# Kernel tuning notes

Measured on AMD Instinct MI355X. Metric: run time of the kernel, lower is better.

## Reference

```python
import jax, jax.numpy as jnp
import numpy as np
from jax import lax

B, C, H, W, D, V = 1, 32, 128, 160, 64, 5


def _make_projs():
    # proj_matrices[b, v, 0] = 4x4 extrinsics [R|t], proj_matrices[b, v, 1] = 4x4 intrinsics
    f = 800.0
    K = np.eye(4, dtype=np.float32)
    K[0, 0] = K[1, 1] = f
    K[0, 2] = W / 2.0
    K[1, 2] = H / 2.0
    projs = np.zeros((B, V, 2, 4, 4), np.float32)
    for b in range(B):
        for v in range(V):
            E = np.eye(4, dtype=np.float32)
            if v > 0:
                ang = 0.02 * v
                ca, sa = np.cos(ang), np.sin(ang)
                E[:3, :3] = np.array([[ca, 0.0, sa], [0.0, 1.0, 0.0], [-sa, 0.0, ca]], np.float32)
                E[:3, 3] = np.array([0.1 * v, 0.02 * v, 0.05 * v], np.float32)
            projs[b, v, 0] = E
            projs[b, v, 1] = K
    return jnp.asarray(projs)


def setup_inputs() -> dict:
    key = jax.random.key(0)
    ks = jax.random.split(key, 6)
    inp = {f"feat{i}": jax.random.normal(ks[i], (B, C, H, W), jnp.float32) for i in range(V)}
    inp["proj_matrices"] = _make_projs()
    inp["depth_values"] = jnp.broadcast_to(
        jnp.linspace(425.0, 935.0, D, dtype=jnp.float32)[None, :], (B, D))
    inp["num_depth"] = D
    inp["conv_w"] = jax.random.normal(ks[5], (1, C, 3, 3, 3), jnp.float32) * 0.05
    inp["conv_b"] = jnp.zeros((1,), jnp.float32)
    return inp


def _bilinear_sample(fea, px, py):
    # fea: [B,C,H,W]; px,py: [B,N] pixel coords. Bilinear, zero padding, align_corners=True.
    Bb, Cc, Hh, Ww = fea.shape
    fea_flat = fea.reshape(Bb, Cc, Hh * Ww)
    x0 = jnp.floor(px)
    y0 = jnp.floor(py)
    wx1 = px - x0
    wy1 = py - y0

    def corner(xc, yc, w):
        valid = (xc >= 0) & (xc <= Ww - 1) & (yc >= 0) & (yc <= Hh - 1)
        xi = jnp.clip(xc, 0, Ww - 1).astype(jnp.int32)
        yi = jnp.clip(yc, 0, Hh - 1).astype(jnp.int32)
        idx = yi * Ww + xi  # [B,N]
        g = jax.vmap(lambda fb, ib: fb[:, ib])(fea_flat, idx)  # [B,C,N]
        return g * (w * valid)[:, None, :]

    return (corner(x0, y0, (1 - wx1) * (1 - wy1))
            + corner(x0 + 1, y0, wx1 * (1 - wy1))
            + corner(x0, y0 + 1, (1 - wx1) * wy1)
            + corner(x0 + 1, y0 + 1, wx1 * wy1))


def _homo_warp(src_fea, src_proj, ref_proj, depth_values):
    # homo_warping_3D: warp src features into ref frustum at each depth hypothesis
    Bb, Cc, Hh, Ww = src_fea.shape
    Dd = depth_values.shape[1]
    proj = jnp.einsum('bij,bjk->bik', src_proj, jnp.linalg.inv(ref_proj))
    rot, trans = proj[:, :3, :3], proj[:, :3, 3]
    yy, xx = jnp.meshgrid(jnp.arange(Hh, dtype=src_fea.dtype),
                          jnp.arange(Ww, dtype=src_fea.dtype), indexing='ij')
    xyz = jnp.stack([xx.ravel(), yy.ravel(), jnp.ones(Hh * Ww, src_fea.dtype)])  # [3,HW]
    rot_xyz = jnp.einsum('bij,jn->bin', rot, xyz)  # [B,3,HW]
    pxyz = rot_xyz[:, :, None, :] * depth_values[:, None, :, None] + trans[:, :, None, None]  # [B,3,D,HW]
    px = (pxyz[:, 0] / pxyz[:, 2]).reshape(Bb, -1)
    py = (pxyz[:, 1] / pxyz[:, 2]).reshape(Bb, -1)
    return _bilinear_sample(src_fea, px, py).reshape(Bb, Cc, Dd, Hh, Ww)


def _fuse_proj(p):
    # p: [B,2,4,4] -> [B,4,4] with K[:3,:3] @ E[:3,:4] written into top 3 rows
    top = jnp.einsum('bij,bjk->bik', p[:, 1, :3, :3], p[:, 0, :3, :4])
    return p[:, 0].at[:, :3, :4].set(top)


def reference(feat0, feat1, feat2, feat3, feat4, proj_matrices, depth_values, num_depth, conv_w, conv_b):
    feats = [feat0, feat1, feat2, feat3, feat4]
    num_views = len(feats)
    Bb, Cc, Hh, Ww = feat0.shape
    ref_proj = _fuse_proj(proj_matrices[:, 0])
    ref_vol = jnp.broadcast_to(feat0[:, :, None, :, :], (Bb, Cc, num_depth, Hh, Ww))
    vol_sum = ref_vol
    vol_sq = ref_vol ** 2
    for v in range(1, num_views):
        src_proj = _fuse_proj(proj_matrices[:, v])
        warped = _homo_warp(feats[v], src_proj, ref_proj, depth_values)
        vol_sum = vol_sum + warped
        vol_sq = vol_sq + warped ** 2
    variance = vol_sq / num_views - (vol_sum / num_views) ** 2  # [B,C,D,H,W]
    cost = lax.conv_general_dilated(variance, conv_w, (1, 1, 1), 'SAME',
                                    dimension_numbers=('NCDHW', 'OIDHW', 'NCDHW'))
    cost = cost + conv_b[None, :, None, None, None]
    prob_volume_pre = cost[:, 0]  # squeeze channel -> [B,D,H,W]
    return jax.nn.softmax(prob_volume_pre, axis=1)
```

## Files before the change

### kernel.cpp

```cpp
#include <hip/hip_runtime.h>

#define H_ 128
#define W_ 160
#define C_ 32
#define D_ 64
#define HW_ (H_*W_)
#define DHW_ (D_*HW_)

#define TY 16
#define TX 16
#define HS 18
#define NP_ (HS*HS)
#define PCHUNK 81

#define GSTR 28

#define FEATT_SZ (5*HW_*C_)
#define MATS_OFF FEATT_SZ
#define CW3_OFF (MATS_OFF + 64)
#define A_OFF (CW3_OFF + 1152)

using v2f = __attribute__((ext_vector_type(2))) float;

__device__ __forceinline__ v2f pk_mul(v2f a, v2f b) {
    v2f d; asm("v_pk_mul_f32 %0, %1, %2" : "=v"(d) : "v"(a), "v"(b)); return d;
}
__device__ __forceinline__ v2f pk_add(v2f a, v2f b) {
    v2f d; asm("v_pk_add_f32 %0, %1, %2" : "=v"(d) : "v"(a), "v"(b)); return d;
}
__device__ __forceinline__ v2f pk_fma(v2f a, v2f b, v2f c) {
    v2f d; asm("v_pk_fma_f32 %0, %1, %2, %3" : "=v"(d) : "v"(a), "v"(b), "v"(c)); return d;
}
__device__ __forceinline__ v2f pk_mul_blo(v2f a, v2f b) {
    v2f d; asm("v_pk_mul_f32 %0, %1, %2 op_sel:[0,0] op_sel_hi:[1,0]" : "=v"(d) : "v"(a), "v"(b)); return d;
}
__device__ __forceinline__ v2f pk_mul_bhi(v2f a, v2f b) {
    v2f d; asm("v_pk_mul_f32 %0, %1, %2 op_sel:[0,1] op_sel_hi:[1,1]" : "=v"(d) : "v"(a), "v"(b)); return d;
}
__device__ __forceinline__ v2f pk_fma_blo(v2f a, v2f b, v2f c) {
    v2f d; asm("v_pk_fma_f32 %0, %1, %2, %3 op_sel:[0,0,0] op_sel_hi:[1,0,1]" : "=v"(d) : "v"(a), "v"(b), "v"(c)); return d;
}
__device__ __forceinline__ v2f pk_fma_bhi(v2f a, v2f b, v2f c) {
    v2f d; asm("v_pk_fma_f32 %0, %1, %2, %3 op_sel:[0,1,0] op_sel_hi:[1,1,1]" : "=v"(d) : "v"(a), "v"(b), "v"(c)); return d;
}
__device__ __forceinline__ v2f pk_fma_alo(v2f a, v2f b, v2f c) {
    v2f d; asm("v_pk_fma_f32 %0, %1, %2, %3 op_sel:[0,0,0] op_sel_hi:[0,1,1]" : "=v"(d) : "v"(a), "v"(b), "v"(c)); return d;
}
__device__ __forceinline__ v2f pk_fma_ahi(v2f a, v2f b, v2f c) {
    v2f d; asm("v_pk_fma_f32 %0, %1, %2, %3 op_sel:[1,0,0] op_sel_hi:[1,1,1]" : "=v"(d) : "v"(a), "v"(b), "v"(c)); return d;
}
__device__ __forceinline__ v2f pk_fma_nsq(v2f a, v2f c) {
    v2f d; asm("v_pk_fma_f32 %0, %1, %1, %2 neg_lo:[1,0,0] neg_hi:[1,0,0]" : "=v"(d) : "v"(a), "v"(c)); return d;
}

__global__ void k_setup(const float* __restrict__ proj,
                        const float* __restrict__ convw,
                        float* __restrict__ mats,
                        float* __restrict__ cw3)
{
    const int tid = threadIdx.x;
    for (int o = tid; o < 1152; o += 64) {
        const int tap = o >> 7;
        const int r   = o & 127;
        const int c   = r >> 2;
        const int kd  = r & 3;
        cw3[o] = (kd < 3) ? convw[c*27 + kd*9 + tap] : 0.f;
    }
    if (tid != 0) return;
    double F[5][12];
    for (int v = 0; v < 5; ++v) {
        const float* E = proj + v*32;
        const float* K = proj + v*32 + 16;
        for (int i = 0; i < 3; ++i)
            for (int j = 0; j < 4; ++j) {
                double s = 0.0;
                for (int k = 0; k < 3; ++k)
                    s += (double)K[i*4+k] * (double)E[k*4+j];
                F[v][i*4+j] = s;
            }
    }
    const double m00=F[0][0], m01=F[0][1], m02=F[0][2],  t0x=F[0][3];
    const double m10=F[0][4], m11=F[0][5], m12=F[0][6],  t0y=F[0][7];
    const double m20=F[0][8], m21=F[0][9], m22=F[0][10], t0z=F[0][11];
    const double det = m00*(m11*m22-m12*m21) - m01*(m10*m22-m12*m20)
                     + m02*(m10*m21-m11*m20);
    const double id = 1.0/det;
    double inv[9];
    inv[0] = (m11*m22-m12*m21)*id; inv[1] = (m02*m21-m01*m22)*id; inv[2] = (m01*m12-m02*m11)*id;
    inv[3] = (m12*m20-m10*m22)*id; inv[4] = (m00*m22-m02*m20)*id; inv[5] = (m02*m10-m00*m12)*id;
    inv[6] = (m10*m21-m11*m20)*id; inv[7] = (m01*m20-m00*m21)*id; inv[8] = (m00*m11-m01*m10)*id;
    double it[3];
    it[0] = -(inv[0]*t0x + inv[1]*t0y + inv[2]*t0z);
    it[1] = -(inv[3]*t0x + inv[4]*t0y + inv[5]*t0z);
    it[2] = -(inv[6]*t0x + inv[7]*t0y + inv[8]*t0z);
    for (int v = 1; v < 5; ++v) {
        float* o = mats + (v-1)*12;
        for (int r = 0; r < 3; ++r) {
            for (int c = 0; c < 3; ++c) {
                double s = 0.0;
                for (int k = 0; k < 3; ++k) s += F[v][r*4+k]*inv[k*3+c];
                o[r*3+c] = (float)s;
            }
            double tr = F[v][r*4+3] + F[v][r*4+0]*it[0]
                      + F[v][r*4+1]*it[1] + F[v][r*4+2]*it[2];
            o[9+r] = (float)tr;
        }
    }
}

__global__ void k_transpose(const float* __restrict__ f0, const float* __restrict__ f1,
                            const float* __restrict__ f2, const float* __restrict__ f3,
                            const float* __restrict__ f4, float* __restrict__ ft)
{
    const int bv = blockIdx.y;
    const float* f = (bv==0) ? f0 : (bv==1) ? f1 : (bv==2) ? f2 : (bv==3) ? f3 : f4;
    float* o = ft + (size_t)bv * (HW_*C_);
    __shared__ float tile[C_][65];
    const int pix0 = blockIdx.x * 64;
    const int tid = threadIdx.x;
    const int p  = tid & 63;
    const int ci = (tid >> 6) * 8;
#pragma unroll
    for (int i = 0; i < 8; ++i)
        tile[ci + i][p] = f[(size_t)(ci + i)*HW_ + pix0 + p];
    __syncthreads();
    const int c2 = tid & 31, pg = tid >> 5;
#pragma unroll
    for (int i = 0; i < 8; ++i) {
        int p2 = pg + i*8;
        o[(size_t)(pix0 + p2)*C_ + c2] = tile[c2][p2];
    }
}

__global__ __launch_bounds__(256, 3) void k_var_conv(
    const float* __restrict__ featT, const float* __restrict__ mats,
    const float* __restrict__ depthv, const float* __restrict__ cw3,
    float* __restrict__ A)
{
    __shared__ float geo[PCHUNK * GSTR];
    __shared__ float vlds[NP_ * C_];
    const int tid = threadIdx.x;
    const int x0 = blockIdx.x * TX;
    const int y0 = blockIdx.y * TY;
    const int bd = blockIdx.z;
    const float depth = depthv[bd];

    const int q = tid & 7;
    const int lane_cb = q << 4;
    const int pg = tid >> 3;
    const char* fT = (const char*)featT;

    for (int chunk = 0; chunk < 4; ++chunk) {
        const int base = chunk * PCHUNK;

        for (int t = tid; t < PCHUNK*4; t += 256) {
            const int pos = t >> 2;
            const int v   = t & 3;
            const int p   = base + pos;
            const int hy = p / HS;
            const int hx = p - hy*HS;
            const int gy = y0 - 1 + hy;
            const int gx = x0 - 1 + hx;
            const bool inimg = ((unsigned)gy < 128u) && ((unsigned)gx < 160u);
            const float fgx = (float)gx, fgy = (float)gy;
            float* gp = geo + pos*GSTR;

            const float* mm = mats + v*12;
            const float c0 = mm[0]*depth, c1 = mm[1]*depth, c2 = fmaf(mm[2], depth, mm[9]);
            const float c3 = mm[3]*depth, c4 = mm[4]*depth, c5 = fmaf(mm[5], depth, mm[10]);
            const float c6 = mm[6]*depth, c7 = mm[7]*depth, c8 = fmaf(mm[8], depth, mm[11]);

            const float xx = fmaf(c0,fgx, fmaf(c1,fgy, c2));
            const float yy = fmaf(c3,fgx, fmaf(c4,fgy, c5));
            const float zz = fmaf(c6,fgx, fmaf(c7,fgy, c8));
            const float rz = __builtin_amdgcn_rcpf(zz);
            const float px = xx*rz, py = yy*rz;
            const float xf = floorf(px), yf = floorf(py);
            const float wx = px - xf, wy = py - yf;
            const int xi = (int)xf, yi = (int)yf;
            const bool vx0 = (xi >=  0) & (xi <= W_-1);
            const bool vx1 = (xi >= -1) & (xi <= W_-2);
            const bool vy0 = (yi >=  0) & (yi <= H_-1);
            const bool vy1 = (yi >= -1) & (yi <= H_-2);
            const int xc0 = min(max(xi,   0), W_-1);
            const int xc1 = min(max(xi+1, 0), W_-1);
            const int yc0 = min(max(yi,   0), H_-1);
            const int yc1 = min(max(yi+1, 0), H_-1);
            const float ux = 1.f - wx, uy = 1.f - wy;
            float4 w4;
            w4.x = (inimg && vx0 && vy0) ? ux*uy : 0.f;
            w4.y = (inimg && vx1 && vy0) ? wx*uy : 0.f;
            w4.z = (inimg && vx0 && vy1) ? ux*wy : 0.f;
            w4.w = (inimg && vx1 && vy1) ? wx*wy : 0.f;
            const int offb00 = (yc0*W_ + xc0) << 7;
            const int dxb    = (xc1 - xc0) << 7;
            const int dyb    = (yc1 - yc0) * 20480;
            *reinterpret_cast<float4*>(gp + v*4) = w4;
            int2 oo; oo.x = offb00; oo.y = dxb | dyb;
            *reinterpret_cast<int2*>(gp + 16 + v*2) = oo;
            if (v == 0) {
                const int gyc = min(max(gy, 0), H_-1);
                const int gxc = min(max(gx, 0), W_-1);
                float2 misc;
                misc.x = __int_as_float((gyc*W_ + gxc) << 7);
                misc.y = inimg ? 1.f : 0.f;
                *reinterpret_cast<float2*>(gp + 24) = misc;
            }
        }
        __syncthreads();

        for (int p = pg; p < PCHUNK; p += 32) {
            const int ap = base + p;
            const float* gp = geo + p*GSTR;
            const float2 misc = *reinterpret_cast<const float2*>(gp + 24);
            v2f misc2 = { misc.x, misc.y };
            const int refoffb = __float_as_int(misc.x) + lane_cb;

            const float4 tr = *reinterpret_cast<const float4*>(fT + refoffb);
            v2f tlo = { tr.x, tr.y }, thi = { tr.z, tr.w };
            v2f s01 = pk_mul_bhi(tlo, misc2);
            v2f s23 = pk_mul_bhi(thi, misc2);
            v2f q01 = pk_mul(s01, tlo);
            v2f q23 = pk_mul(s23, thi);

#pragma unroll
            for (int v = 0; v < 4; ++v) {
                const float4 w4 = *reinterpret_cast<const float4*>(gp + v*4);
                const int2  oo = *reinterpret_cast<const int2*>(gp + 16 + v*2);
                const int v00 = oo.x + lane_cb;
                const int dx  = oo.y & 128;
                const int dy  = oo.y - dx;
                const char* fb = fT + (size_t)(v+1)*(HW_*C_*4);
                const float4 t00 = *reinterpret_cast<const float4*>(fb + v00);
                const float4 t10 = *reinterpret_cast<const float4*>(fb + (v00 + dx));
                const float4 t01 = *reinterpret_cast<const float4*>(fb + (v00 + dy));
                const float4 t11 = *reinterpret_cast<const float4*>(fb + (v00 + dx + dy));
                v2f w01 = { w4.x, w4.y }, w23 = { w4.z, w4.w };
                v2f a;
                a = pk_mul_blo((v2f){t00.x,t00.y}, w01);
                a = pk_fma_bhi((v2f){t10.x,t10.y}, w01, a);
                a = pk_fma_blo((v2f){t01.x,t01.y}, w23, a);
                a = pk_fma_bhi((v2f){t11.x,t11.y}, w23, a);
                s01 = pk_add(s01, a);
                q01 = pk_fma(a, a, q01);
                v2f b;
                b = pk_mul_blo((v2f){t00.z,t00.w}, w01);
                b = pk_fma_bhi((v2f){t10.z,t10.w}, w01, b);
                b = pk_fma_blo((v2f){t01.z,t01.w}, w23, b);
                b = pk_fma_bhi((v2f){t11.z,t11.w}, w23, b);
                s23 = pk_add(s23, b);
                q23 = pk_fma(b, b, q23);
            }
            const v2f c5 = { 0.2f, 0.2f };
            v2f m01 = pk_mul(s01, c5), m23 = pk_mul(s23, c5);
            v2f o01 = pk_fma_nsq(m01, pk_mul(q01, c5));
            v2f o23 = pk_fma_nsq(m23, pk_mul(q23, c5));
            float4 ov = make_float4(o01.x, o01.y, o23.x, o23.y);
            *reinterpret_cast<float4*>(vlds + ap*C_ + ((q ^ (ap & 7)) << 2)) = ov;
        }
        __syncthreads();
    }

    const int oy = tid >> 4;
    const int ox = tid & 15;
    v2f acc01 = { 0.f, 0.f };
    float acc2 = 0.f;
#pragma unroll
    for (int ky = 0; ky < 3; ++ky) {
#pragma unroll
        for (int kx = 0; kx < 3; ++kx) {
            const int p = (oy+ky)*HS + (ox+kx);
            const int sw = p & 7;
            const float* wt   = cw3 + (ky*3+kx)*128;
            const float* vrow = vlds + p*C_;
#pragma unroll
            for (int cq = 0; cq < 8; ++cq) {
                const float4 dv = *reinterpret_cast<const float4*>(vrow + ((cq^sw)<<2));
                const float* wc = wt + cq*16;
                v2f d01 = { dv.x, dv.y }, d23 = { dv.z, dv.w };
                const float2 wk0 = *reinterpret_cast<const float2*>(wc + 0);
                const float2 wk1 = *reinterpret_cast<const float2*>(wc + 4);
                const float2 wk2 = *reinterpret_cast<const float2*>(wc + 8);
                const float2 wk3 = *reinterpret_cast<const float2*>(wc + 12);
                acc01 = pk_fma_alo(d01, (v2f){wk0.x, wk0.y}, acc01);
                acc01 = pk_fma_ahi(d01, (v2f){wk1.x, wk1.y}, acc01);
                acc01 = pk_fma_alo(d23, (v2f){wk2.x, wk2.y}, acc01);
                acc01 = pk_fma_ahi(d23, (v2f){wk3.x, wk3.y}, acc01);
                acc2 = fmaf(dv.x, wc[2],  acc2);
                acc2 = fmaf(dv.y, wc[6],  acc2);
                acc2 = fmaf(dv.z, wc[10], acc2);
                acc2 = fmaf(dv.w, wc[14], acc2);
            }
        }
    }
    const size_t o = (size_t)bd*HW_ + (size_t)(y0+oy)*W_ + (x0+ox);
    A[o]                    = acc01.x;
    A[(size_t)DHW_ + o]     = acc01.y;
    A[2*(size_t)DHW_ + o]   = acc2;
}

__global__ void k_softmax(const float* __restrict__ A,
                          const float* __restrict__ conv_b,
                          float* __restrict__ out)
{
    const int pix = blockIdx.x*256 + threadIdx.x;
    const float bs = conv_b[0];
    float cst[D_];
#pragma unroll
    for (int d = 0; d < D_; ++d) {
        float v = A[(size_t)DHW_ + (size_t)d*HW_ + pix];
        if (d > 0)      v += A[(size_t)(d-1)*HW_ + pix];
        if (d < D_-1)   v += A[2*(size_t)DHW_ + (size_t)(d+1)*HW_ + pix];
        cst[d] = v + bs;
    }
    float m = cst[0];
#pragma unroll
    for (int d = 1; d < D_; ++d) m = fmaxf(m, cst[d]);
    float s = 0.f;
#pragma unroll
    for (int d = 0; d < D_; ++d) { cst[d] = expf(cst[d] - m); s += cst[d]; }
    const float rs = 1.0f / s;
#pragma unroll
    for (int d = 0; d < D_; ++d)
        out[(size_t)d*HW_ + pix] = cst[d]*rs;
}

extern "C" void kernel_launch(void* const* d_in, const int* in_sizes, int n_in,
                              void* d_out, int out_size, void* d_ws, size_t ws_size,
                              hipStream_t stream)
{
    const float* proj   = (const float*)d_in[5];
    const float* depth  = (const float*)d_in[6];
    const float* conv_w = (const float*)d_in[8];
    const float* conv_b = (const float*)d_in[9];

    float* ws    = (float*)d_ws;
    float* featT = ws;
    float* mats  = ws + MATS_OFF;
    float* cw3   = ws + CW3_OFF;
    float* A     = ws + A_OFF;

    k_setup<<<1, 64, 0, stream>>>(proj, conv_w, mats, cw3);
    dim3 gt(HW_/64, 5);
    k_transpose<<<gt, 256, 0, stream>>>((const float*)d_in[0], (const float*)d_in[1],
                                        (const float*)d_in[2], (const float*)d_in[3],
                                        (const float*)d_in[4], featT);
    dim3 g1(W_/TX, H_/TY, D_);
    k_var_conv<<<g1, 256, 0, stream>>>(featT, mats, depth, cw3, A);
    k_softmax<<<HW_/256, 256, 0, stream>>>(A, conv_b, (float*)d_out);
}
```

Baseline: 207.7 us.

## Shrink var-conv tile to 16x8 with smaller LDS and split conv channels across lane pairs

Halves the output tile height so the halo and the variance LDS buffer shrink, and packs the geometry record into fewer words (offset plus two flag bits), so more blocks fit per CU (launch bounds raised to 6). Sampling now runs in 6 chunks of 32 halo pixels with one pass per chunk. The 3x3x3 conv splits the 32 channels between lane pairs and combines the partial sums with a shuffle. The cost is a larger relative halo overhead (18x10 for 128 outputs), twice as many blocks, more barriers per block, and idle threads in the chunk loops.

Measured after the change: 604.6 us. +191.1%, slower.

```diff
diff --git a/kernel.cpp b/kernel.cpp
--- a/kernel.cpp
+++ b/kernel.cpp
@@ -7,13 +7,15 @@
 #define HW_ (H_*W_)
 #define DHW_ (D_*HW_)
 
-#define TY 16
 #define TX 16
-#define HS 18
-#define NP_ (HS*HS)
-#define PCHUNK 81
-
-#define GSTR 28
+#define TY 8
+#define HX 18
+#define HYR 10
+#define NP_ (HX*HYR)
+#define PCH 32
+#define NCH 6
+
+#define GSTR 24
 
 #define FEATT_SZ (5*HW_*C_)
 #define MATS_OFF FEATT_SZ
@@ -132,12 +134,12 @@
     }
 }
 
-__global__ __launch_bounds__(256, 3) void k_var_conv(
+__global__ __launch_bounds__(256, 6) void k_var_conv(
     const float* __restrict__ featT, const float* __restrict__ mats,
     const float* __restrict__ depthv, const float* __restrict__ cw3,
     float* __restrict__ A)
 {
-    __shared__ float geo[PCHUNK * GSTR];
+    __shared__ float geo[PCH * GSTR];
     __shared__ float vlds[NP_ * C_];
     const int tid = threadIdx.x;
     const int x0 = blockIdx.x * TX;
@@ -147,18 +149,18 @@
 
     const int q = tid & 7;
     const int lane_cb = q << 4;
-    const int pg = tid >> 3;
     const char* fT = (const char*)featT;
 
-    for (int chunk = 0; chunk < 4; ++chunk) {
-        const int base = chunk * PCHUNK;
-
-        for (int t = tid; t < PCHUNK*4; t += 256) {
-            const int pos = t >> 2;
-            const int v   = t & 3;
+    for (int c = 0; c < NCH; ++c) {
+        const int base = c * PCH;
+        const int n = (base + PCH <= NP_) ? PCH : (NP_ - base);
+
+        if (tid < n*4) {
+            const int pos = tid >> 2;
+            const int v   = tid & 3;
             const int p   = base + pos;
-            const int hy = p / HS;
-            const int hx = p - hy*HS;
+            const int hy = p / HX;
+            const int hx = p - hy*HX;
             const int gy = y0 - 1 + hy;
             const int gx = x0 - 1 + hx;
             const bool inimg = ((unsigned)gy < 128u) && ((unsigned)gx < 160u);
@@ -192,29 +194,27 @@
             w4.y = (inimg && vx1 && vy0) ? wx*uy : 0.f;
             w4.z = (inimg && vx0 && vy1) ? ux*wy : 0.f;
             w4.w = (inimg && vx1 && vy1) ? wx*wy : 0.f;
-            const int offb00 = (yc0*W_ + xc0) << 7;
-            const int dxb    = (xc1 - xc0) << 7;
-            const int dyb    = (yc1 - yc0) * 20480;
+            const unsigned offb00 = (unsigned)((yc0*W_ + xc0) << 7);
+            const unsigned pk = offb00 | ((unsigned)(xc1 - xc0) << 30)
+                                       | ((unsigned)(yc1 - yc0) << 31);
             *reinterpret_cast<float4*>(gp + v*4) = w4;
-            int2 oo; oo.x = offb00; oo.y = dxb | dyb;
-            *reinterpret_cast<int2*>(gp + 16 + v*2) = oo;
+            *reinterpret_cast<unsigned*>(gp + 16 + v) = pk;
             if (v == 0) {
                 const int gyc = min(max(gy, 0), H_-1);
                 const int gxc = min(max(gx, 0), W_-1);
-                float2 misc;
-                misc.x = __int_as_float((gyc*W_ + gxc) << 7);
-                misc.y = inimg ? 1.f : 0.f;
-                *reinterpret_cast<float2*>(gp + 24) = misc;
+                *reinterpret_cast<int*>(gp + 20) = (gyc*W_ + gxc) << 7;
+                gp[21] = inimg ? 1.f : 0.f;
             }
         }
         __syncthreads();
 
-        for (int p = pg; p < PCHUNK; p += 32) {
-            const int ap = base + p;
-            const float* gp = geo + p*GSTR;
-            const float2 misc = *reinterpret_cast<const float2*>(gp + 24);
-            v2f misc2 = { misc.x, misc.y };
-            const int refoffb = __float_as_int(misc.x) + lane_cb;
+        if (tid < n*8) {
+            const int pos = tid >> 3;
+            const int ap = base + pos;
+            const float* gp = geo + pos*GSTR;
+            const int refoffb = *reinterpret_cast<const int*>(gp + 20) + lane_cb;
+            const float vp = gp[21];
+            v2f misc2 = { 0.f, vp };
 
             const float4 tr = *reinterpret_cast<const float4*>(fT + refoffb);
             v2f tlo = { tr.x, tr.y }, thi = { tr.z, tr.w };
@@ -226,10 +226,10 @@
 #pragma unroll
             for (int v = 0; v < 4; ++v) {
                 const float4 w4 = *reinterpret_cast<const float4*>(gp + v*4);
-                const int2  oo = *reinterpret_cast<const int2*>(gp + 16 + v*2);
-                const int v00 = oo.x + lane_cb;
-                const int dx  = oo.y & 128;
-                const int dy  = oo.y - dx;
+                const unsigned pk = *reinterpret_cast<const unsigned*>(gp + 16 + v);
+                const int v00 = (int)(pk & 0x00FFFFFFu) + lane_cb;
+                const int dx  = (pk & 0x40000000u) ? 128 : 0;
+                const int dy  = (pk & 0x80000000u) ? 20480 : 0;
                 const char* fb = fT + (size_t)(v+1)*(HW_*C_*4);
                 const float4 t00 = *reinterpret_cast<const float4*>(fb + v00);
                 const float4 t10 = *reinterpret_cast<const float4*>(fb + (v00 + dx));
@@ -261,22 +261,25 @@
         __syncthreads();
     }
 
-    const int oy = tid >> 4;
-    const int ox = tid & 15;
+    const int outp = tid >> 1;
+    const int half = tid & 1;
+    const int oy = outp >> 4;
+    const int ox = outp & 15;
     v2f acc01 = { 0.f, 0.f };
     float acc2 = 0.f;
 #pragma unroll
     for (int ky = 0; ky < 3; ++ky) {
 #pragma unroll
         for (int kx = 0; kx < 3; ++kx) {
-            const int p = (oy+ky)*HS + (ox+kx);
+            const int p = (oy+ky)*HX + (ox+kx);
             const int sw = p & 7;
             const float* wt   = cw3 + (ky*3+kx)*128;
             const float* vrow = vlds + p*C_;
 #pragma unroll
-            for (int cq = 0; cq < 8; ++cq) {
-                const float4 dv = *reinterpret_cast<const float4*>(vrow + ((cq^sw)<<2));
-                const float* wc = wt + cq*16;
+            for (int cq2 = 0; cq2 < 4; ++cq2) {
+                const int qq = half*4 + cq2;
+                const float4 dv = *reinterpret_cast<const float4*>(vrow + ((qq^sw)<<2));
+                const float* wc = wt + qq*16;
                 v2f d01 = { dv.x, dv.y }, d23 = { dv.z, dv.w };
                 const float2 wk0 = *reinterpret_cast<const float2*>(wc + 0);
                 const float2 wk1 = *reinterpret_cast<const float2*>(wc + 4);
@@ -293,10 +296,15 @@
             }
         }
     }
-    const size_t o = (size_t)bd*HW_ + (size_t)(y0+oy)*W_ + (x0+ox);
-    A[o]                    = acc01.x;
-    A[(size_t)DHW_ + o]     = acc01.y;
-    A[2*(size_t)DHW_ + o]   = acc2;
+    float a0 = acc01.x + __shfl_xor(acc01.x, 1, 64);
+    float a1 = acc01.y + __shfl_xor(acc01.y, 1, 64);
+    float a2 = acc2    + __shfl_xor(acc2,    1, 64);
+    if (half == 0) {
+        const size_t o = (size_t)bd*HW_ + (size_t)(y0+oy)*W_ + (x0+ox);
+        A[o]                    = a0;
+        A[(size_t)DHW_ + o]     = a1;
+        A[2*(size_t)DHW_ + o]   = a2;
+    }
 }
 
 __global__ void k_softmax(const float* __restrict__ A,
```
